# Kernel tuning notes

Hardware: AMD Instinct MI355X
Metric: run time of the kernel (lower is better)

Reference implementation:

```python
import jax, jax.numpy as jnp
import numpy as np

B, T, D, H = 2, 2048, 2048, 16
HS = D // H  # head size 128


def setup_inputs() -> dict:
    key = jax.random.key(0)
    ks = jax.random.split(key, 5)
    s = 0.02
    return {
        "x": jax.random.normal(ks[0], (B, T, D), dtype=jnp.float32),
        "wq": jax.random.normal(ks[1], (D, D), dtype=jnp.float32) * s,
        "wk": jax.random.normal(ks[2], (D, D), dtype=jnp.float32) * s,
        "wv": jax.random.normal(ks[3], (D, D), dtype=jnp.float32) * s,
        "wo": jax.random.normal(ks[4], (D, D), dtype=jnp.float32) * s,
    }


def reference(x, wq, wk, wv, wo):
    b, t, d = x.shape
    # projections: nn.Linear(x) = x @ W.T ; here W stored as (out,in)
    q = (x @ wq.T).reshape(b, t, H, HS).transpose(0, 2, 1, 3)  # (B,H,T,HS)
    k = (x @ wk.T).reshape(b, t, H, HS).transpose(0, 2, 1, 3)
    v = (x @ wv.T).reshape(b, t, H, HS).transpose(0, 2, 1, 3)
    scale = 1.0 / np.sqrt(HS).astype(np.float32)
    e = jnp.einsum("bhqd,bhkd->bhqk", q, k) * scale  # (B,H,T,T)
    causal = jnp.tril(jnp.ones((t, t), dtype=bool))
    e = jnp.where(causal[None, None], e, jnp.float32(-jnp.inf))
    alpha = jax.nn.softmax(e, axis=-1)  # dropout=0.0 -> identity
    attn = jnp.einsum("bhqk,bhkd->bhqd", alpha, v)
    attn = attn.transpose(0, 2, 1, 3).reshape(b, t, d)
    return attn @ wo.T
```

## Files before the change

kernel.cpp:

```cpp
#include <hip/hip_runtime.h>
#include <hip/hip_bf16.h>

typedef __bf16 bf16x8 __attribute__((ext_vector_type(8)));
typedef float f32x4 __attribute__((ext_vector_type(4)));
typedef unsigned short u16x8 __attribute__((ext_vector_type(8)));

#define GLDS16(g, s)                                                         \
  __builtin_amdgcn_global_load_lds(                                          \
      (const __attribute__((address_space(1))) void*)(g),                    \
      (__attribute__((address_space(3))) void*)(s), 16, 0, 0)

__device__ __forceinline__ void store1(__hip_bfloat16* p, float v) { *p = __float2bfloat16(v); }
__device__ __forceinline__ void store1(float* p, float v) { *p = v; }

__global__ __launch_bounds__(256) void cast_f32_to_bf16(const float4* __restrict__ in,
                                                        ushort4* __restrict__ out, int n4) {
  int i = blockIdx.x * 256 + threadIdx.x;
  if (i >= n4) return;
  float4 v = in[i];
  union { ushort4 u; __hip_bfloat16 h[4]; } o;
  o.h[0] = __float2bfloat16(v.x);
  o.h[1] = __float2bfloat16(v.y);
  o.h[2] = __float2bfloat16(v.z);
  o.h[3] = __float2bfloat16(v.w);
  out[i] = o.u;
}

__global__ __launch_bounds__(256) void cast4_f32_to_bf16(const float4* __restrict__ w0,
                                                         const float4* __restrict__ w1,
                                                         const float4* __restrict__ w2,
                                                         const float4* __restrict__ w3,
                                                         ushort4* __restrict__ o0,
                                                         ushort4* __restrict__ o1,
                                                         ushort4* __restrict__ o2,
                                                         ushort4* __restrict__ o3, int n4) {
  int i = blockIdx.x * 256 + threadIdx.x;
  if (i >= n4) return;
  int s = blockIdx.y;
  const float4* in = (s == 0) ? w0 : (s == 1) ? w1 : (s == 2) ? w2 : w3;
  ushort4* out = (s == 0) ? o0 : (s == 1) ? o1 : (s == 2) ? o2 : o3;
  float4 v = in[i];
  union { ushort4 u; __hip_bfloat16 h[4]; } o;
  o.h[0] = __float2bfloat16(v.x);
  o.h[1] = __float2bfloat16(v.y);
  o.h[2] = __float2bfloat16(v.z);
  o.h[3] = __float2bfloat16(v.w);
  out[i] = o.u;
}

template <typename OutT>
__global__ __launch_bounds__(512, 2) void gemm256(const __hip_bfloat16* __restrict__ A,
                                                  const __hip_bfloat16* __restrict__ B0,
                                                  const __hip_bfloat16* __restrict__ B1,
                                                  const __hip_bfloat16* __restrict__ B2,
                                                  OutT* __restrict__ C0,
                                                  OutT* __restrict__ C1,
                                                  OutT* __restrict__ C2,
                                                  int nBx, int nBy, int ntPerMat,
                                                  int N, int K) {
  __shared__ __hip_bfloat16 As[3][128 * 64];
  __shared__ __hip_bfloat16 Bs[3][256 * 64];

  const int t = threadIdx.x;
  const int w = t >> 6, l = t & 63;
  const int lr = l & 15, hi = l >> 4;

  const int nwg = nBx * nBy;
  int id = (int)blockIdx.x;
  id = (id & 7) * (nwg >> 3) + (id >> 3);
  const int bx = id / nBy;
  const int by = id % nBy;

  const int sel = bx / ntPerMat;
  const __hip_bfloat16* Bm = (sel == 0) ? B0 : ((sel == 1) ? B1 : B2);
  OutT* Cm = (sel == 0) ? C0 : ((sel == 1) ? C1 : C2);
  const int n0 = (bx - sel * ntPerMat) * 256;
  const int m0 = by * 128;

  const int c0r = t >> 3, cs = t & 7;
  const int c1r = 64 + c0r;
  const __hip_bfloat16* aP0 = A + (size_t)(m0 + c0r) * K + (cs ^ (c0r & 7)) * 8;
  const __hip_bfloat16* aP1 = A + (size_t)(m0 + c1r) * K + (cs ^ (c1r & 7)) * 8;
  const __hip_bfloat16* bP0 = Bm + (size_t)(n0 + c0r) * K + (cs ^ (c0r & 7)) * 8;
  const __hip_bfloat16* bP1 = Bm + (size_t)(n0 + c1r) * K + (cs ^ (c1r & 7)) * 8;
  const size_t HK = (size_t)128 * K;

#define STAGE_T(bb, koff)                                                    \
  do {                                                                       \
    GLDS16(aP0 + (koff), (char*)As[bb] + t * 16);                            \
    GLDS16(aP1 + (koff), (char*)As[bb] + 8192 + t * 16);                     \
    GLDS16(bP0 + (koff), (char*)Bs[bb] + t * 16);                            \
    GLDS16(bP1 + (koff), (char*)Bs[bb] + 8192 + t * 16);                     \
    GLDS16(bP0 + HK + (koff), (char*)Bs[bb] + 16384 + t * 16);               \
    GLDS16(bP1 + HK + (koff), (char*)Bs[bb] + 24576 + t * 16);               \
  } while (0)

  f32x4 acc[2][4][2] = {};
  bf16x8 afA[4][2];
  bf16x8 bqA[2][2], bqB[2][2];
  const int NT = K / 64;
  const int sw = lr & 7;
  const int arow = (w >> 2) * 64;
  const int brow = (w & 3) * 32;

#define RD_A(dst)                                                            \
  _Pragma("unroll") for (int mi = 0; mi < 4; ++mi)                           \
    _Pragma("unroll") for (int kk = 0; kk < 2; ++kk)                         \
      dst[mi][kk] = *(const bf16x8*)((const char*)As[buf] +                  \
          (arow + mi * 16 + lr) * 128 + (((kk * 4 + hi) ^ sw) << 4));
#define RD_B(dst, nh)                                                        \
  _Pragma("unroll") for (int ni = 0; ni < 2; ++ni)                           \
    _Pragma("unroll") for (int kk = 0; kk < 2; ++kk)                         \
      dst[ni][kk] = *(const bf16x8*)((const char*)Bs[buf] +                  \
          ((nh) * 128 + brow + ni * 16 + lr) * 128 + (((kk * 4 + hi) ^ sw) << 4));
#define MFMA_Q(nh, afv, bq)                                                  \
  do {                                                                       \
    __builtin_amdgcn_s_setprio(1);                                           \
    _Pragma("unroll") for (int mi = 0; mi < 4; ++mi)                         \
      _Pragma("unroll") for (int ni = 0; ni < 2; ++ni) {                     \
        acc[nh][mi][ni] = __builtin_amdgcn_mfma_f32_16x16x32_bf16(           \
            afv[mi][0], bq[ni][0], acc[nh][mi][ni], 0, 0, 0);                \
        acc[nh][mi][ni] = __builtin_amdgcn_mfma_f32_16x16x32_bf16(           \
            afv[mi][1], bq[ni][1], acc[nh][mi][ni], 0, 0, 0);                \
      }                                                                      \
    __builtin_amdgcn_s_setprio(0);                                           \
  } while (0)
#define WAITV(n)  asm volatile("s_waitcnt vmcnt(" #n ")" ::: "memory")

  STAGE_T(0, 0);
  STAGE_T(1, 64);

  for (int tt = 0; tt < NT; ++tt) {
    const int buf = tt % 3;

    if (tt + 1 < NT) WAITV(6); else WAITV(0);
    __builtin_amdgcn_s_barrier();

    RD_A(afA);
    RD_B(bqA, 0);
    RD_B(bqB, 1);
    if (tt + 2 < NT) STAGE_T((tt + 2) % 3, (size_t)(tt + 2) * 64);

    MFMA_Q(0, afA, bqA);
    MFMA_Q(1, afA, bqB);
  }
#undef WAITV
#undef MFMA_Q
#undef RD_B
#undef RD_A
#undef STAGE_T

#pragma unroll
  for (int nh = 0; nh < 2; ++nh)
#pragma unroll
    for (int mi = 0; mi < 4; ++mi)
#pragma unroll
      for (int ni = 0; ni < 2; ++ni)
#pragma unroll
        for (int i = 0; i < 4; ++i) {
          size_t idx = (size_t)(m0 + arow + mi * 16 + hi * 4 + i) * N +
                       (n0 + nh * 128 + brow + ni * 16 + lr);
          store1(&Cm[idx], acc[nh][mi][ni][i]);
        }
}

__global__ __launch_bounds__(256, 2) void flash_attn(const __hip_bfloat16* __restrict__ Qg,
                                                     const __hip_bfloat16* __restrict__ Kg,
                                                     const __hip_bfloat16* __restrict__ Vg,
                                                     __hip_bfloat16* __restrict__ Og) {
  __shared__ __hip_bfloat16 Ks[2][64 * 128];
  __shared__ __hip_bfloat16 Vt[128 * 64];

  const int mblk = blockIdx.x;
  const int bh = mblk & 31;
  const int jj = mblk >> 5;
  const int qt = (jj < 8) ? (15 - jj) : (jj - 8);
  const int b = bh >> 4, h = bh & 15;
  const int q0 = qt * 128;
  const int t = threadIdx.x, w = t >> 6, l = t & 63;
  const int lr = l & 15, hi = l >> 4;
  const size_t base = ((size_t)b * 2048) * 2048 + (size_t)h * 128;
  const int nt = 2 * qt + 2;
  const float scale = 0.08838834764831843f;

  const int hi2 = (hi & 1) * 2;
  const int addrA = (((hi2) << 4) | lr) << 2;
  const int addrB = (((hi2 + 1) << 4) | lr) << 2;
  int addr_o[4];
#pragma unroll
  for (int i = 0; i < 4; ++i) addr_o[i] = ((l & 48) | (hi * 4 + i)) << 2;
  const bool hiHigh = (hi >> 1) != 0;

  bf16x8 qf[2][4];
#pragma unroll
  for (int g = 0; g < 2; ++g) {
    const __hip_bfloat16* qrow = Qg + base + (size_t)(q0 + w * 32 + g * 16 + lr) * 2048;
#pragma unroll
    for (int kk = 0; kk < 4; ++kk)
      qf[g][kk] = *(const bf16x8*)(qrow + kk * 32 + hi * 8);
  }

  f32x4 o_acc[2][8] = {};
  float m_run[2] = {-1e30f, -1e30f};
  float l_run[2] = {0.f, 0.f};

  const __hip_bfloat16* kptr[4];
#pragma unroll
  for (int i = 0; i < 4; ++i) {
    int c = i * 256 + t;
    int kr = c >> 4;
    int ke = ((c & 15) ^ (kr & 7)) * 8;
    kptr[i] = Kg + base + (size_t)kr * 2048 + ke;
  }
  const __hip_bfloat16* vptr[2];
#pragma unroll
  for (int it = 0; it < 2; ++it) {
    int kp = it * 16 + w * 4 + hi;
    vptr[it] = Vg + base + (size_t)(kp * 2) * 2048 + lr * 8;
  }

  u16x8 va[2], vb[2];
#pragma unroll
  for (int i = 0; i < 4; ++i)
    GLDS16(kptr[i], (char*)Ks[0] + (i * 256 + t) * 16);
#pragma unroll
  for (int it = 0; it < 2; ++it) {
    va[it] = *(const u16x8*)vptr[it];
    vb[it] = *(const u16x8*)(vptr[it] + 2048);
  }

  for (int kt = 0; kt < nt; ++kt) {
    const int cur = kt & 1;
    const int kb = kt * 64;
    __syncthreads();

#pragma unroll
    for (int it = 0; it < 2; ++it)
#pragma unroll
      for (int j2 = 0; j2 < 8; ++j2) {
        int d = lr * 8 + j2;
        int sw = (lr ^ j2) & 7;
        int off = d * 128 + (((it * 4 + w) ^ sw) << 4) + hi * 4;
        *(unsigned int*)((char*)Vt + off) =
            (unsigned int)va[it][j2] | ((unsigned int)vb[it][j2] << 16);
      }
    if (kt + 1 < nt) {
      const size_t adv = (size_t)(kb + 64) * 2048;
#pragma unroll
      for (int i = 0; i < 4; ++i)
        GLDS16(kptr[i] + adv, (char*)Ks[cur ^ 1] + (i * 256 + t) * 16);
#pragma unroll
      for (int it = 0; it < 2; ++it) {
        va[it] = *(const u16x8*)(vptr[it] + adv);
        vb[it] = *(const u16x8*)(vptr[it] + adv + 2048);
      }
    }
    asm volatile("s_waitcnt lgkmcnt(0)" ::: "memory");
    __builtin_amdgcn_s_barrier();

    if (!(kt == nt - 1 && w < 2)) {
      const char* ks = (const char*)Ks[cur];

      f32x4 st[2][4];
#pragma unroll
      for (int g = 0; g < 2; ++g)
#pragma unroll
        for (int nk = 0; nk < 4; ++nk) { f32x4 z = {}; st[g][nk] = z; }
#pragma unroll
      for (int nk = 0; nk < 4; ++nk)
#pragma unroll
        for (int kk = 0; kk < 4; ++kk) {
          bf16x8 kf = *(const bf16x8*)(ks + (nk * 16 + lr) * 256 +
                                       (((kk * 4 + hi) ^ (lr & 7)) << 4));
#pragma unroll
          for (int g = 0; g < 2; ++g)
            st[g][nk] = __builtin_amdgcn_mfma_f32_16x16x32_bf16(kf, qf[g][kk], st[g][nk], 0, 0, 0);
        }

      const bool maskt = (kt >= nt - 2);
#pragma unroll
      for (int g = 0; g < 2; ++g)
#pragma unroll
        for (int nk = 0; nk < 4; ++nk)
#pragma unroll
          for (int i = 0; i < 4; ++i) {
            float v = st[g][nk][i] * scale;
            if (maskt) {
              int ki = kb + nk * 16 + hi * 4 + i;
              int qi = q0 + w * 32 + g * 16 + lr;
              if (ki > qi) v = -1e30f;
            }
            st[g][nk][i] = v;
          }

      bf16x8 paf[2][2];
#pragma unroll
      for (int g = 0; g < 2; ++g) {
        float t0 = fmaxf(fmaxf(st[g][0][0], st[g][0][1]), fmaxf(st[g][0][2], st[g][0][3]));
        float t1 = fmaxf(fmaxf(st[g][1][0], st[g][1][1]), fmaxf(st[g][1][2], st[g][1][3]));
        float t2 = fmaxf(fmaxf(st[g][2][0], st[g][2][1]), fmaxf(st[g][2][2], st[g][2][3]));
        float t3 = fmaxf(fmaxf(st[g][3][0], st[g][3][1]), fmaxf(st[g][3][2], st[g][3][3]));
        float mx = fmaxf(fmaxf(t0, t1), fmaxf(t2, t3));
        mx = fmaxf(mx, __shfl_xor(mx, 16));
        mx = fmaxf(mx, __shfl_xor(mx, 32));

        if (!__all(mx - m_run[g] <= 8.0f)) {
          float mnew = fmaxf(m_run[g], mx);
          float rs = __expf(m_run[g] - mnew);
          m_run[g] = mnew;
          l_run[g] *= rs;
          int rsi = __float_as_int(rs);
#pragma unroll
          for (int i = 0; i < 4; ++i) {
            float rso = __int_as_float(__builtin_amdgcn_ds_bpermute(addr_o[i], rsi));
#pragma unroll
            for (int nc = 0; nc < 8; ++nc) o_acc[g][nc][i] *= rso;
          }
        }

#pragma unroll
        for (int nk = 0; nk < 4; ++nk)
#pragma unroll
          for (int i = 0; i < 4; ++i)
            st[g][nk][i] = __expf(st[g][nk][i] - m_run[g]);

        float s0 = (st[g][0][0] + st[g][0][1]) + (st[g][0][2] + st[g][0][3]);
        float s1 = (st[g][1][0] + st[g][1][1]) + (st[g][1][2] + st[g][1][3]);
        float s2 = (st[g][2][0] + st[g][2][1]) + (st[g][2][2] + st[g][2][3]);
        float s3 = (st[g][3][0] + st[g][3][1]) + (st[g][3][2] + st[g][3][3]);
        float sm = (s0 + s1) + (s2 + s3);
        sm += __shfl_xor(sm, 16);
        sm += __shfl_xor(sm, 32);
        l_run[g] += sm;

        unsigned pk[4][2];
#pragma unroll
        for (int nk = 0; nk < 4; ++nk) {
          asm("v_cvt_pk_bf16_f32 %0, %1, %2"
              : "=v"(pk[nk][0]) : "v"(st[g][nk][0]), "v"(st[g][nk][1]));
          asm("v_cvt_pk_bf16_f32 %0, %1, %2"
              : "=v"(pk[nk][1]) : "v"(st[g][nk][2]), "v"(st[g][nk][3]));
        }

#pragma unroll
        for (int kk = 0; kk < 2; ++kk) {
          unsigned au[4];
#pragma unroll
          for (int p = 0; p < 4; ++p) {
            int ad = (p < 2) ? addrA : addrB;
            int v0 = __builtin_amdgcn_ds_bpermute(ad, (int)pk[2 * kk][p & 1]);
            int v1 = __builtin_amdgcn_ds_bpermute(ad, (int)pk[2 * kk + 1][p & 1]);
            au[p] = hiHigh ? (unsigned)v1 : (unsigned)v0;
          }
          union { unsigned u[4]; bf16x8 v; } cv;
          cv.u[0] = au[0]; cv.u[1] = au[1]; cv.u[2] = au[2]; cv.u[3] = au[3];
          paf[g][kk] = cv.v;
        }
      }

#pragma unroll
      for (int kk = 0; kk < 2; ++kk)
#pragma unroll
        for (int nc = 0; nc < 8; ++nc) {
          int d = nc * 16 + lr;
          int sw = ((d >> 3) ^ d) & 7;
          bf16x8 vfr = *(const bf16x8*)((const char*)Vt + d * 128 +
                                        (((kk * 4 + hi) ^ sw) << 4));
#pragma unroll
          for (int g = 0; g < 2; ++g)
            o_acc[g][nc] = __builtin_amdgcn_mfma_f32_16x16x32_bf16(paf[g][kk], vfr, o_acc[g][nc], 0, 0, 0);
        }
    }
  }

#pragma unroll
  for (int g = 0; g < 2; ++g) {
    float lo[4];
#pragma unroll
    for (int i = 0; i < 4; ++i)
      lo[i] = __int_as_float(__builtin_amdgcn_ds_bpermute(addr_o[i], __float_as_int(l_run[g])));
#pragma unroll
    for (int nc = 0; nc < 8; ++nc)
#pragma unroll
      for (int i = 0; i < 4; ++i) {
        float val = o_acc[g][nc][i] / lo[i];
        Og[base + (size_t)(q0 + w * 32 + g * 16 + hi * 4 + i) * 2048 + nc * 16 + lr] =
            __float2bfloat16(val);
      }
  }
}

extern "C" void kernel_launch(void* const* d_in, const int* in_sizes, int n_in,
                              void* d_out, int out_size, void* d_ws, size_t ws_size,
                              hipStream_t stream) {
  const float* x  = (const float*)d_in[0];
  const float* wq = (const float*)d_in[1];
  const float* wk = (const float*)d_in[2];
  const float* wv = (const float*)d_in[3];
  const float* wo = (const float*)d_in[4];
  float* out = (float*)d_out;

  const int BT = 4096, D = 2048;
  const size_t ND = (size_t)D * D;
  const size_t NX = (size_t)BT * D;

  __hip_bfloat16* xb  = (__hip_bfloat16*)d_ws;
  __hip_bfloat16* wqb = xb + NX;
  __hip_bfloat16* wkb = wqb + ND;
  __hip_bfloat16* wvb = wkb + ND;
  __hip_bfloat16* wob = wvb + ND;
  __hip_bfloat16* Qb  = wob + ND;
  __hip_bfloat16* Kb  = Qb + NX;
  __hip_bfloat16* Vb  = Kb + NX;
  __hip_bfloat16* Ab  = Vb + NX;

  cast_f32_to_bf16<<<(int)(NX / 4 / 256), 256, 0, stream>>>((const float4*)x, (ushort4*)xb, (int)(NX / 4));
  cast4_f32_to_bf16<<<dim3((int)(ND / 4 / 256), 4), 256, 0, stream>>>(
      (const float4*)wq, (const float4*)wk, (const float4*)wv, (const float4*)wo,
      (ushort4*)wqb, (ushort4*)wkb, (ushort4*)wvb, (ushort4*)wob, (int)(ND / 4));

  gemm256<__hip_bfloat16><<<768, 512, 0, stream>>>(
      xb, wqb, wkb, wvb, Qb, Kb, Vb, 24, 32, 8, D, D);

  flash_attn<<<512, 256, 0, stream>>>(Qb, Kb, Vb, Ab);

  gemm256<float><<<256, 512, 0, stream>>>(
      Ab, wob, wob, wob, out, out, out, 8, 32, 8, D, D);
}
```

Measured before the change: 277.6 us.

## Fuse QKV projection into one kernel sharing A tile across three weight matrices

```diff
diff --git a/kernel.cpp b/kernel.cpp
--- a/kernel.cpp
+++ b/kernel.cpp
@@ -48,18 +48,16 @@
   out[i] = o.u;
 }
 
-template <typename OutT>
-__global__ __launch_bounds__(512, 2) void gemm256(const __hip_bfloat16* __restrict__ A,
-                                                  const __hip_bfloat16* __restrict__ B0,
-                                                  const __hip_bfloat16* __restrict__ B1,
-                                                  const __hip_bfloat16* __restrict__ B2,
-                                                  OutT* __restrict__ C0,
-                                                  OutT* __restrict__ C1,
-                                                  OutT* __restrict__ C2,
-                                                  int nBx, int nBy, int ntPerMat,
-                                                  int N, int K) {
-  __shared__ __hip_bfloat16 As[3][128 * 64];
-  __shared__ __hip_bfloat16 Bs[3][256 * 64];
+__global__ __launch_bounds__(512, 2) void gemm_qkv3(const __hip_bfloat16* __restrict__ A,
+                                                    const __hip_bfloat16* __restrict__ B0,
+                                                    const __hip_bfloat16* __restrict__ B1,
+                                                    const __hip_bfloat16* __restrict__ B2,
+                                                    __hip_bfloat16* __restrict__ C0,
+                                                    __hip_bfloat16* __restrict__ C1,
+                                                    __hip_bfloat16* __restrict__ C2,
+                                                    int nBx, int nBy, int N, int K) {
+  __shared__ __hip_bfloat16 As[2][128 * 64];
+  __shared__ __hip_bfloat16 Bs[2][3][128 * 64];
 
   const int t = threadIdx.x;
   const int w = t >> 6, l = t & 63;
@@ -71,18 +69,124 @@
   const int bx = id / nBy;
   const int by = id % nBy;
 
-  const int sel = bx / ntPerMat;
-  const __hip_bfloat16* Bm = (sel == 0) ? B0 : ((sel == 1) ? B1 : B2);
-  OutT* Cm = (sel == 0) ? C0 : ((sel == 1) ? C1 : C2);
-  const int n0 = (bx - sel * ntPerMat) * 256;
+  const int n0 = bx * 128;
+  const int m0 = by * 128;
+
+  const int c0r = t >> 3, cs = t & 7;
+  const int c1r = 64 + c0r;
+  const size_t aoff0 = (size_t)(m0 + c0r) * K + (cs ^ (c0r & 7)) * 8;
+  const size_t aoff1 = (size_t)(m0 + c1r) * K + (cs ^ (c1r & 7)) * 8;
+  const size_t boff0 = (size_t)(n0 + c0r) * K + (cs ^ (c0r & 7)) * 8;
+  const size_t boff1 = (size_t)(n0 + c1r) * K + (cs ^ (c1r & 7)) * 8;
+
+#define STAGE_T(bb, koff)                                                    \
+  do {                                                                       \
+    GLDS16(A + aoff0 + (koff), (char*)As[bb] + t * 16);                      \
+    GLDS16(A + aoff1 + (koff), (char*)As[bb] + 8192 + t * 16);               \
+    GLDS16(B0 + boff0 + (koff), (char*)Bs[bb][0] + t * 16);                  \
+    GLDS16(B0 + boff1 + (koff), (char*)Bs[bb][0] + 8192 + t * 16);           \
+    GLDS16(B1 + boff0 + (koff), (char*)Bs[bb][1] + t * 16);                  \
+    GLDS16(B1 + boff1 + (koff), (char*)Bs[bb][1] + 8192 + t * 16);           \
+    GLDS16(B2 + boff0 + (koff), (char*)Bs[bb][2] + t * 16);                  \
+    GLDS16(B2 + boff1 + (koff), (char*)Bs[bb][2] + 8192 + t * 16);           \
+  } while (0)
+
+  f32x4 acc[3][4][2] = {};
+  bf16x8 af[4][2];
+  const int NT = K / 64;
+  const int sw = lr & 7;
+  const int arow = (w >> 2) * 64;
+  const int brow = (w & 3) * 32;
+
+#define WAITV(n)  asm volatile("s_waitcnt vmcnt(" #n ")" ::: "memory")
+
+  STAGE_T(0, 0);
+
+  for (int tt = 0; tt < NT; ++tt) {
+    const int buf = tt & 1, nb = buf ^ 1;
+    const bool stg = (tt + 1 < NT);
+    const size_t ko = (size_t)(tt + 1) * 64;
+
+    WAITV(0);
+    __builtin_amdgcn_s_barrier();
+
+#pragma unroll
+    for (int mi = 0; mi < 4; ++mi)
+#pragma unroll
+      for (int kk = 0; kk < 2; ++kk)
+        af[mi][kk] = *(const bf16x8*)((const char*)As[buf] +
+            (arow + mi * 16 + lr) * 128 + (((kk * 4 + hi) ^ sw) << 4));
+
+    if (stg) STAGE_T(nb, ko);
+
+#pragma unroll
+    for (int m = 0; m < 3; ++m) {
+      bf16x8 bq[2][2];
+#pragma unroll
+      for (int ni = 0; ni < 2; ++ni)
+#pragma unroll
+        for (int kk = 0; kk < 2; ++kk)
+          bq[ni][kk] = *(const bf16x8*)((const char*)Bs[buf][m] +
+              (brow + ni * 16 + lr) * 128 + (((kk * 4 + hi) ^ sw) << 4));
+      __builtin_amdgcn_s_setprio(1);
+#pragma unroll
+      for (int mi = 0; mi < 4; ++mi)
+#pragma unroll
+        for (int ni = 0; ni < 2; ++ni) {
+          acc[m][mi][ni] = __builtin_amdgcn_mfma_f32_16x16x32_bf16(
+              af[mi][0], bq[ni][0], acc[m][mi][ni], 0, 0, 0);
+          acc[m][mi][ni] = __builtin_amdgcn_mfma_f32_16x16x32_bf16(
+              af[mi][1], bq[ni][1], acc[m][mi][ni], 0, 0, 0);
+        }
+      __builtin_amdgcn_s_setprio(0);
+    }
+  }
+#undef WAITV
+#undef STAGE_T
+
+#pragma unroll
+  for (int m = 0; m < 3; ++m) {
+    __hip_bfloat16* Cm = (m == 0) ? C0 : (m == 1) ? C1 : C2;
+#pragma unroll
+    for (int mi = 0; mi < 4; ++mi)
+#pragma unroll
+      for (int ni = 0; ni < 2; ++ni)
+#pragma unroll
+        for (int i = 0; i < 4; ++i) {
+          size_t idx = (size_t)(m0 + arow + mi * 16 + hi * 4 + i) * N +
+                       (n0 + brow + ni * 16 + lr);
+          store1(&Cm[idx], acc[m][mi][ni][i]);
+        }
+  }
+}
+
+template <typename OutT>
+__global__ __launch_bounds__(512, 2) void gemm256(const __hip_bfloat16* __restrict__ A,
+                                                  const __hip_bfloat16* __restrict__ B0,
+                                                  OutT* __restrict__ C0,
+                                                  int nBx, int nBy, int N, int K) {
+  __shared__ __hip_bfloat16 As[2][128 * 64];
+  __shared__ __hip_bfloat16 Bs[2][256 * 64];
+
+  const int t = threadIdx.x;
+  const int w = t >> 6, l = t & 63;
+  const int lr = l & 15, hi = l >> 4;
+
+  const int nwg = nBx * nBy;
+  int id = (int)blockIdx.x;
+  id = (id & 7) * (nwg >> 3) + (id >> 3);
+  const int bx = id / nBy;
+  const int by = id % nBy;
+
+  const int n0 = bx * 256;
   const int m0 = by * 128;
 
   const int c0r = t >> 3, cs = t & 7;
   const int c1r = 64 + c0r;
   const __hip_bfloat16* aP0 = A + (size_t)(m0 + c0r) * K + (cs ^ (c0r & 7)) * 8;
   const __hip_bfloat16* aP1 = A + (size_t)(m0 + c1r) * K + (cs ^ (c1r & 7)) * 8;
-  const __hip_bfloat16* bP0 = Bm + (size_t)(n0 + c0r) * K + (cs ^ (c0r & 7)) * 8;
-  const __hip_bfloat16* bP1 = Bm + (size_t)(n0 + c1r) * K + (cs ^ (c1r & 7)) * 8;
+  const __hip_bfloat16* bP0 = B0 + (size_t)(n0 + c0r) * K + (cs ^ (c0r & 7)) * 8;
+  const __hip_bfloat16* bP1 = B0 + (size_t)(n0 + c1r) * K + (cs ^ (c1r & 7)) * 8;
   const size_t HK = (size_t)128 * K;
 
 #define STAGE_T(bb, koff)                                                    \
@@ -128,19 +232,18 @@
 #define WAITV(n)  asm volatile("s_waitcnt vmcnt(" #n ")" ::: "memory")
 
   STAGE_T(0, 0);
-  STAGE_T(1, 64);
 
   for (int tt = 0; tt < NT; ++tt) {
-    const int buf = tt % 3;
-
-    if (tt + 1 < NT) WAITV(6); else WAITV(0);
+    const int buf = tt & 1, nb = buf ^ 1;
+    const bool stg = (tt + 1 < NT);
+    const size_t ko = (size_t)(tt + 1) * 64;
+
+    WAITV(0);
     __builtin_amdgcn_s_barrier();
-
     RD_A(afA);
     RD_B(bqA, 0);
     RD_B(bqB, 1);
-    if (tt + 2 < NT) STAGE_T((tt + 2) % 3, (size_t)(tt + 2) * 64);
-
+    if (stg) STAGE_T(nb, ko);
     MFMA_Q(0, afA, bqA);
     MFMA_Q(1, afA, bqB);
   }
@@ -160,7 +263,7 @@
         for (int i = 0; i < 4; ++i) {
           size_t idx = (size_t)(m0 + arow + mi * 16 + hi * 4 + i) * N +
                        (n0 + nh * 128 + brow + ni * 16 + lr);
-          store1(&Cm[idx], acc[nh][mi][ni][i]);
+          store1(&C0[idx], acc[nh][mi][ni][i]);
         }
 }
 
@@ -419,11 +522,9 @@
       (const float4*)wq, (const float4*)wk, (const float4*)wv, (const float4*)wo,
       (ushort4*)wqb, (ushort4*)wkb, (ushort4*)wvb, (ushort4*)wob, (int)(ND / 4));
 
-  gemm256<__hip_bfloat16><<<768, 512, 0, stream>>>(
-      xb, wqb, wkb, wvb, Qb, Kb, Vb, 24, 32, 8, D, D);
+  gemm_qkv3<<<512, 512, 0, stream>>>(xb, wqb, wkb, wvb, Qb, Kb, Vb, 16, 32, D, D);
 
   flash_attn<<<512, 256, 0, stream>>>(Qb, Kb, Vb, Ab);
 
-  gemm256<float><<<256, 512, 0, stream>>>(
-      Ab, wob, wob, wob, out, out, out, 8, 32, 8, D, D);
+  gemm256<float><<<256, 512, 0, stream>>>(Ab, wob, out, 8, 32, D, D);
 }
```

Result: no change. 274.6 us (-1.1%).
